# Performance work log

Measured on AMD Instinct MI355X. Metric: run time of the kernel, lower is better.

Reference implementation:

```python
import jax, jax.numpy as jnp
import numpy as np

NEG_SLOPE = 0.01  # nn.LeakyReLU default


def layer_norm(x, g, b, eps=1e-5):
    mu = x.mean(-1, keepdims=True)
    var = x.var(-1, keepdims=True)
    return (x - mu) / jnp.sqrt(var + eps) * g + b


def gru_layer(x, W_ih, W_hh, b_ih, b_hh):
    # x: (N, T, in). PyTorch GRU gate order: r, z, n.
    N, T, _ = x.shape
    H = W_hh.shape[1]
    xg = x @ W_ih.T + b_ih              # (N, T, 3H), input projections precomputed
    xg = jnp.transpose(xg, (1, 0, 2))   # (T, N, 3H)

    def step(h, xt):
        hg = h @ W_hh.T + b_hh
        xr, xz, xn = jnp.split(xt, 3, axis=-1)
        hr, hz, hn = jnp.split(hg, 3, axis=-1)
        r = jax.nn.sigmoid(xr + hr)
        z = jax.nn.sigmoid(xz + hz)
        n = jnp.tanh(xn + r * hn)
        h = (1.0 - z) * n + z * h
        return h, h

    h0 = jnp.zeros((N, H), x.dtype)
    _, ys = jax.lax.scan(step, h0, xg)  # (T, N, H)
    return jnp.transpose(ys, (1, 0, 2))


def prior_hconv(xW, Hinc):
    # PyG HypergraphConv: out = D_n^{-1} H B_e^{-1} H^T (x W^T); diag norms as vector scales
    d_n = Hinc.sum(1)
    d_e = Hinc.sum(0)
    inv_dn = jnp.where(d_n > 0, 1.0 / d_n, 0.0)
    inv_de = jnp.where(d_e > 0, 1.0 / d_e, 0.0)
    m = (Hinc.T @ xW) * inv_de[:, None]  # (E, H) hyperedge aggregation
    return (Hinc @ m) * inv_dn[:, None]


def soft_hconv(xW, Hinc):
    # SoftHypergraphConv: D_n^{-1/2} H D_e^{-1} H^T (x W^T + b)
    d_n = Hinc.sum(1)
    d_e = Hinc.sum(0)
    inv_sqrt_dn = jnp.where(d_n > 0, 1.0 / jnp.sqrt(d_n), 0.0)
    inv_de = jnp.where(d_e > 0, 1.0 / d_e, 0.0)
    m = (Hinc.T @ xW) * inv_de[:, None]
    return (Hinc @ m) * inv_sqrt_dn[:, None]


def setup_inputs() -> dict:
    key = jax.random.key(0)
    N, T, F, H, K, E = 4000, 64, 128, 128, 32, 64
    ks = jax.random.split(key, 20)
    s = 0.05
    inp = {
        'x': jax.random.normal(ks[0], (N, T, F), jnp.float32),
        'industry_matrix': jax.random.randint(ks[1], (N, E), 0, 2, jnp.int32),
        'ln_g': jnp.ones((F,), jnp.float32),
        'ln_b': jnp.zeros((F,), jnp.float32),
        'W_ih0': jax.random.normal(ks[2], (3 * H, F), jnp.float32) * s,
        'W_hh0': jax.random.normal(ks[3], (3 * H, H), jnp.float32) * s,
        'b_ih0': jax.random.normal(ks[4], (3 * H,), jnp.float32) * s,
        'b_hh0': jax.random.normal(ks[5], (3 * H,), jnp.float32) * s,
        'W_ih1': jax.random.normal(ks[6], (3 * H, H), jnp.float32) * s,
        'W_hh1': jax.random.normal(ks[7], (3 * H, H), jnp.float32) * s,
        'b_ih1': jax.random.normal(ks[8], (3 * H,), jnp.float32) * s,
        'b_hh1': jax.random.normal(ks[9], (3 * H,), jnp.float32) * s,
        'Wp': jax.random.normal(ks[10], (H, H), jnp.float32) * s,
        'bp': jax.random.normal(ks[11], (H,), jnp.float32) * s,
        'prototypes': jax.random.normal(ks[12], (K, H), jnp.float32),
        'Ws': jax.random.normal(ks[13], (H, H), jnp.float32) * s,
        'bs': jax.random.normal(ks[14], (H,), jnp.float32) * s,
        'Wa': jax.random.normal(ks[15], (H, H), jnp.float32) * s,
        'ba': jax.random.normal(ks[16], (H,), jnp.float32) * s,
        'Wf': jax.random.normal(ks[17], (1, 3 * H), jnp.float32) * s,
        'bf': jax.random.normal(ks[18], (1,), jnp.float32) * s,
    }
    return inp


def reference(x, industry_matrix, ln_g, ln_b, W_ih0, W_hh0, b_ih0, b_hh0,
              W_ih1, W_hh1, b_ih1, b_hh1, Wp, bp, prototypes, Ws, bs,
              Wa, ba, Wf, bf):
    lrelu = lambda v: jax.nn.leaky_relu(v, NEG_SLOPE)
    # FeatureExtractor: LN -> 2-layer GRU -> last timestep (linear branch is discarded in source)
    xn = layer_norm(x, ln_g, ln_b)
    h1 = gru_layer(xn, W_ih0, W_hh0, b_ih0, b_hh0)
    h2 = gru_layer(h1, W_ih1, W_hh1, b_ih1, b_hh1)
    e_s = h2[:, -1, :]                                   # (N, H)
    # PriorBetaModule: PyG HypergraphConv on binary industry incidence
    Hp = industry_matrix.astype(e_s.dtype)               # (N, E) 0/1 incidence
    e_p = lrelu(prior_hconv(e_s @ Wp.T, Hp) + bp)
    e_r = e_s - e_p
    # HiddenBetaModule: soft incidence via prototypes
    beta_h = jax.nn.sigmoid(e_r @ prototypes.T)          # (N, K)
    e_h = lrelu(soft_hconv(e_r @ Ws.T + bs, beta_h))
    e_residual = e_r - e_h
    e_alpha = lrelu(e_residual @ Wa.T + ba)
    out = jnp.concatenate([e_p, e_h, e_alpha], axis=1) @ Wf.T + bf
    return out.reshape(-1)                               # (N,)
```

## Files before the change

### kernel.cpp

```cpp
#include <hip/hip_runtime.h>
#include <hip/hip_fp16.h>

typedef float    f32x4 __attribute__((ext_vector_type(4)));
typedef _Float16 f16x8 __attribute__((ext_vector_type(8)));

__device__ __forceinline__ float sigmoidf_(float x) { return __builtin_amdgcn_rcpf(1.f + __expf(-x)); }
__device__ __forceinline__ float tanhf_(float x) { float e = __expf(2.f * x); return 1.f - 2.f * __builtin_amdgcn_rcpf(e + 1.f); }
__device__ __forceinline__ float lrelu_(float v) { return v > 0.f ? v : 0.01f * v; }

__device__ __forceinline__ f16x8 cvt8(const float* p) {
    const f32x4* q = (const f32x4*)p;
    f32x4 a = q[0], b = q[1];
    f16x8 v;
    v[0] = (_Float16)a[0]; v[1] = (_Float16)a[1]; v[2] = (_Float16)a[2]; v[3] = (_Float16)a[3];
    v[4] = (_Float16)b[0]; v[5] = (_Float16)b[1]; v[6] = (_Float16)b[2]; v[7] = (_Float16)b[3];
    return v;
}

__device__ __forceinline__ void gload_lds16(const void* g, void* l) {
    __builtin_amdgcn_global_load_lds(
        (const __attribute__((address_space(1))) void*)g,
        (__attribute__((address_space(3))) void*)l,
        16, 0, 0);
}

__global__ __launch_bounds__(256) void k_ln(const float* __restrict__ x,
                                            const float* __restrict__ g,
                                            const float* __restrict__ b,
                                            _Float16* __restrict__ xn, int N)
{
    int tid = threadIdx.x;
    int r = tid >> 4, i = tid & 15;
    size_t row = (size_t)blockIdx.x * 16 + r;
    int n = (int)(row >> 6), t = (int)(row & 63);
    const f32x4* xp = (const f32x4*)(x + row * 128 + i * 8);
    f32x4 a0 = xp[0], a1 = xp[1];
    float v0=a0[0], v1=a0[1], v2=a0[2], v3=a0[3], v4=a1[0], v5=a1[1], v6=a1[2], v7=a1[3];
    float s  = v0+v1+v2+v3+v4+v5+v6+v7;
    float s2 = v0*v0+v1*v1+v2*v2+v3*v3+v4*v4+v5*v5+v6*v6+v7*v7;
#pragma unroll
    for (int m = 1; m <= 8; m <<= 1) { s += __shfl_xor(s, m); s2 += __shfl_xor(s2, m); }
    float mu  = s * (1.f / 128.f);
    float var = s2 * (1.f / 128.f) - mu * mu;
    float rs  = rsqrtf(var + 1e-5f);
    const f32x4* gp = (const f32x4*)(g + i * 8);
    const f32x4* bp = (const f32x4*)(b + i * 8);
    f32x4 g0 = gp[0], g1 = gp[1], bb0 = bp[0], bb1 = bp[1];
    f16x8 o;
    o[0] = (_Float16)((v0 - mu) * rs * g0[0] + bb0[0]);
    o[1] = (_Float16)((v1 - mu) * rs * g0[1] + bb0[1]);
    o[2] = (_Float16)((v2 - mu) * rs * g0[2] + bb0[2]);
    o[3] = (_Float16)((v3 - mu) * rs * g0[3] + bb0[3]);
    o[4] = (_Float16)((v4 - mu) * rs * g1[0] + bb1[0]);
    o[5] = (_Float16)((v5 - mu) * rs * g1[1] + bb1[1]);
    o[6] = (_Float16)((v6 - mu) * rs * g1[2] + bb1[2]);
    o[7] = (_Float16)((v7 - mu) * rs * g1[3] + bb1[3]);
    *(f16x8*)(xn + ((size_t)t * N + n) * 128 + i * 8) = o;
}

__global__ __launch_bounds__(512) __attribute__((amdgpu_waves_per_eu(2)))
void k_gru2(const _Float16* __restrict__ xin,
            const float* __restrict__ W_ih0,
            const float* __restrict__ W_hh0,
            const float* __restrict__ b_ih0,
            const float* __restrict__ b_hh0,
            const float* __restrict__ W_ih1,
            const float* __restrict__ W_hh1,
            const float* __restrict__ b_ih1,
            const float* __restrict__ b_hh1,
            float* __restrict__ es, int N)
{
    __shared__ __align__(16) _Float16 wlds[96 * 64 * 8];
    __shared__ __align__(16) _Float16 wldsr[32 * 64 * 8];
    __shared__ __align__(16) _Float16 hbuf0[2][16 * 136];
    __shared__ __align__(16) _Float16 hbuf1[2][16 * 136];
    __shared__ __align__(16) _Float16 xls[2][16 * 128];

    int tid = threadIdx.x;
    int w = tid >> 6, lane = tid & 63;
    int ul = lane & 15, q = lane >> 4;
    int u = w * 16 + ul;
    int n0 = blockIdx.x * 16;

#pragma unroll
    for (int g = 0; g < 3; ++g)
#pragma unroll
        for (int kt = 0; kt < 4; ++kt) {
            f16x8 v = cvt8(W_ih0 + (size_t)(u + g * 128) * 128 + kt * 32 + q * 8);
            *(f16x8*)&wlds[(size_t)((w * 12 + g * 4 + kt) * 64 + lane) * 8] = v;
        }
#pragma unroll
    for (int kt = 0; kt < 4; ++kt) {
        f16x8 v = cvt8(W_hh0 + (size_t)u * 128 + kt * 32 + q * 8);
        *(f16x8*)&wldsr[(size_t)((w * 4 + kt) * 64 + lane) * 8] = v;
    }
    const _Float16* wbase  = &wlds[(size_t)(w * 12 * 64 + lane) * 8];
    const _Float16* w0base = &wldsr[(size_t)(w * 4 * 64 + lane) * 8];

    f16x8 whh0zn[8], wih1[12], whh1[12];
#pragma unroll
    for (int kt = 0; kt < 4; ++kt) {
        whh0zn[kt]     = cvt8(W_hh0 + (size_t)(u + 128) * 128 + kt * 32 + q * 8);
        whh0zn[4 + kt] = cvt8(W_hh0 + (size_t)(u + 256) * 128 + kt * 32 + q * 8);
    }
#pragma unroll
    for (int g = 0; g < 3; ++g)
#pragma unroll
        for (int kt = 0; kt < 4; ++kt) {
            size_t roff = (size_t)(u + g * 128) * 128 + kt * 32 + q * 8;
            wih1[g * 4 + kt] = cvt8(W_ih1 + roff);
            whh1[g * 4 + kt] = cvt8(W_hh1 + roff);
        }
    float br0 = b_ih0[u] + b_hh0[u], bz0 = b_ih0[u + 128] + b_hh0[u + 128];
    float bin0 = b_ih0[u + 256], bhn0 = b_hh0[u + 256];
    float br1 = b_ih1[u] + b_hh1[u], bz1 = b_ih1[u + 128] + b_hh1[u + 128];
    float bin1 = b_ih1[u + 256], bhn1 = b_hh1[u + 256];

    for (int idx = tid; idx < 16 * 136; idx += 512) {
        hbuf0[0][idx] = (_Float16)0.f;
        hbuf1[0][idx] = (_Float16)0.f;
        hbuf1[1][idx] = (_Float16)0.f;
    }
    float h0j[4] = {0.f, 0.f, 0.f, 0.f}, h1j[4] = {0.f, 0.f, 0.f, 0.f};
    const f32x4 Z4 = {0.f, 0.f, 0.f, 0.f};

    int xoff[4];
#pragma unroll
    for (int kt = 0; kt < 4; ++kt)
        xoff[kt] = (ul * 256 + kt * 64 + q * 16) ^ ((ul & 7) << 4);
    int dlin = w * 1024 + (lane << 4);
    int dsrc = dlin ^ (((dlin >> 8) & 7) << 4);

#define PREF_X(T, PB)                                                                \
    if (w < 4) {                                                                     \
        const char* gsrc = (const char*)(xin + ((size_t)(T) * N + n0) * 128);        \
        gload_lds16(gsrc + dsrc, (void*)((char*)&xls[PB][0] + dlin));                \
    }

#define LOAD_HF(HF, BUF, PB)                                                         \
    { const _Float16* hb = &BUF[PB][ul * 136 + q * 8];                               \
      _Pragma("unroll")                                                              \
      for (int kt = 0; kt < 4; ++kt) HF[kt] = *(const f16x8*)(hb + kt * 32); }

#define L0_KT(KT, XB)                                                                \
    {                                                                                \
        f16x8 xv  = *(const f16x8*)((XB) + xoff[KT]);                                \
        f16x8 wrv = *(const f16x8*)(wbase + (size_t)(KT) * 512);                     \
        f16x8 wzv = *(const f16x8*)(wbase + (size_t)(4 + (KT)) * 512);               \
        f16x8 wnv = *(const f16x8*)(wbase + (size_t)(8 + (KT)) * 512);               \
        f16x8 w0r = *(const f16x8*)(w0base + (size_t)(KT) * 512);                    \
        ar0  = __builtin_amdgcn_mfma_f32_16x16x32_f16(xv, wrv, ar0, 0, 0, 0);        \
        ar0  = __builtin_amdgcn_mfma_f32_16x16x32_f16(h0f[KT], w0r, ar0, 0, 0, 0);   \
        az0  = __builtin_amdgcn_mfma_f32_16x16x32_f16(xv, wzv, az0, 0, 0, 0);        \
        az0  = __builtin_amdgcn_mfma_f32_16x16x32_f16(h0f[KT], whh0zn[KT], az0, 0, 0, 0); \
        an0x = __builtin_amdgcn_mfma_f32_16x16x32_f16(xv, wnv, an0x, 0, 0, 0);       \
        an0h = __builtin_amdgcn_mfma_f32_16x16x32_f16(h0f[KT], whh0zn[4 + (KT)], an0h, 0, 0, 0); \
    }

#define L1_KT(KT)                                                                    \
    {                                                                                \
        ar1  = __builtin_amdgcn_mfma_f32_16x16x32_f16(h0f[KT], wih1[KT], ar1, 0, 0, 0); \
        ar1  = __builtin_amdgcn_mfma_f32_16x16x32_f16(h1f[KT], whh1[KT], ar1, 0, 0, 0); \
        az1  = __builtin_amdgcn_mfma_f32_16x16x32_f16(h0f[KT], wih1[4 + (KT)], az1, 0, 0, 0); \
        az1  = __builtin_amdgcn_mfma_f32_16x16x32_f16(h1f[KT], whh1[4 + (KT)], az1, 0, 0, 0); \
        an1x = __builtin_amdgcn_mfma_f32_16x16x32_f16(h0f[KT], wih1[8 + (KT)], an1x, 0, 0, 0); \
        an1h = __builtin_amdgcn_mfma_f32_16x16x32_f16(h1f[KT], whh1[8 + (KT)], an1h, 0, 0, 0); \
    }

#define GATES_L0(PW)                                                                 \
    { _Float16* wb = &hbuf0[PW][0];                                                  \
      _Pragma("unroll")                                                              \
      for (int j = 0; j < 4; ++j) {                                                  \
          float rr = sigmoidf_(ar0[j] + br0);                                        \
          float zz = sigmoidf_(az0[j] + bz0);                                        \
          float nn = tanhf_(an0x[j] + bin0 + rr * (an0h[j] + bhn0));                 \
          float hn = (1.f - zz) * nn + zz * h0j[j];                                  \
          h0j[j] = hn;                                                               \
          wb[(q * 4 + j) * 136 + u] = (_Float16)hn;                                  \
      } }

#define GATES_L1(PW)                                                                 \
    { _Float16* wb = &hbuf1[PW][0];                                                  \
      _Pragma("unroll")                                                              \
      for (int j = 0; j < 4; ++j) {                                                  \
          float rr = sigmoidf_(ar1[j] + br1);                                        \
          float zz = sigmoidf_(az1[j] + bz1);                                        \
          float nn = tanhf_(an1x[j] + bin1 + rr * (an1h[j] + bhn1));                 \
          float hn = (1.f - zz) * nn + zz * h1j[j];                                  \
          h1j[j] = hn;                                                               \
          wb[(q * 4 + j) * 136 + u] = (_Float16)hn;                                  \
      } }

    PREF_X(0, 0);
    __syncthreads();

    {
        PREF_X(1, 1);
        f16x8 h0f[4];
        LOAD_HF(h0f, hbuf0, 0);
        f32x4 ar0 = Z4, az0 = Z4, an0x = Z4, an0h = Z4;
        const char* xb = (const char*)&xls[0][0];
        L0_KT(0, xb) L0_KT(1, xb) L0_KT(2, xb) L0_KT(3, xb)
        GATES_L0(1);
        __syncthreads();
    }

    for (int s = 1; s < 64; ++s) {
        int P = s & 1;
        if (s < 63) { PREF_X(s + 1, P ^ 1); }
        f16x8 h0f[4], h1f[4];
        LOAD_HF(h0f, hbuf0, P);
        LOAD_HF(h1f, hbuf1, P);
        f32x4 ar0 = Z4, az0 = Z4, an0x = Z4, an0h = Z4;
        f32x4 ar1 = Z4, az1 = Z4, an1x = Z4, an1h = Z4;
        const char* xb = (const char*)&xls[P][0];
        L0_KT(0, xb) L1_KT(0)
        L0_KT(1, xb) L1_KT(1)
        L0_KT(2, xb) L1_KT(2)
        L0_KT(3, xb) L1_KT(3)
        GATES_L0(P ^ 1);
        GATES_L1(P ^ 1);
        __syncthreads();
    }

    {
        f16x8 h0f[4], h1f[4];
        LOAD_HF(h0f, hbuf0, 0);
        LOAD_HF(h1f, hbuf1, 0);
        f32x4 ar1 = Z4, az1 = Z4, an1x = Z4, an1h = Z4;
        L1_KT(0) L1_KT(1) L1_KT(2) L1_KT(3)
#pragma unroll
        for (int j = 0; j < 4; ++j) {
            float rr = sigmoidf_(ar1[j] + br1);
            float zz = sigmoidf_(az1[j] + bz1);
            float nn = tanhf_(an1x[j] + bin1 + rr * (an1h[j] + bhn1));
            h1j[j] = (1.f - zz) * nn + zz * h1j[j];
        }
    }

#pragma unroll
    for (int j = 0; j < 4; ++j)
        es[(size_t)(n0 + q * 4 + j) * 128 + u] = h1j[j];

#undef PREF_X
#undef LOAD_HF
#undef L0_KT
#undef L1_KT
#undef GATES_L0
#undef GATES_L1
}

#define STAGE_W(SRC)                                                                  \
    _Pragma("unroll")                                                                 \
    for (int tile = 0; tile < 2; ++tile)                                              \
    _Pragma("unroll")                                                                 \
    for (int kt = 0; kt < 4; ++kt) {                                                  \
        f16x8 v = cvt8((SRC) + (size_t)(w * 32 + tile * 16 + ul) * 128 + kt * 32 + q * 8); \
        *(f16x8*)&wfr[(size_t)(((w * 2 + tile) * 4 + kt) * 64 + lane) * 8] = v;       \
    }

#define LOAD_AF(AF, TF)                                                               \
    _Pragma("unroll")                                                                 \
    for (int kt = 0; kt < 4; ++kt) AF[kt] = cvt8(&TF[ul][kt * 32 + q * 8]);

#define MM128T(AF, A0, A1)                                                            \
    _Pragma("unroll")                                                                 \
    for (int kt = 0; kt < 4; ++kt) {                                                  \
        f16x8 b0 = *(const f16x8*)&wfr[(size_t)(((w * 2 + 0) * 4 + kt) * 64 + lane) * 8]; \
        f16x8 b1 = *(const f16x8*)&wfr[(size_t)(((w * 2 + 1) * 4 + kt) * 64 + lane) * 8]; \
        A0 = __builtin_amdgcn_mfma_f32_16x16x32_f16(AF[kt], b0, A0, 0, 0, 0);         \
        A1 = __builtin_amdgcn_mfma_f32_16x16x32_f16(AF[kt], b1, A1, 0, 0, 0);         \
    }

#define STAGE_ROWS16(DST, SRC)                                                        \
    { int r_ = tid >> 4, i_ = tid & 15;                                               \
      const f32x4* sp_ = (const f32x4*)((SRC) + (size_t)(n0 + r_) * 128 + i_ * 8);    \
      f32x4 a_ = sp_[0], b_ = sp_[1];                                                 \
      *(f32x4*)&DST[r_][i_ * 8] = a_;                                                 \
      *(f32x4*)&DST[r_][i_ * 8 + 4] = b_; }

__global__ __launch_bounds__(256) void k_postA(
    const float* __restrict__ e_s, const int* __restrict__ Hp,
    const float* __restrict__ Wp,
    float* __restrict__ macc_e, float* __restrict__ d_e)
{
    __shared__ __align__(16) _Float16 wfr[32 * 64 * 8];
    __shared__ float esf[16][132], xwf[16][132];
    int tid = threadIdx.x;
    int w = tid >> 6, lane = tid & 63;
    int ul = lane & 15, q = lane >> 4;
    int n0 = blockIdx.x * 16;
    const f32x4 Z4 = {0.f, 0.f, 0.f, 0.f};

    STAGE_W(Wp);
    STAGE_ROWS16(esf, e_s);
    __syncthreads();
    {
        f16x8 af[4]; LOAD_AF(af, esf);
        f32x4 a0 = Z4, a1 = Z4;
        MM128T(af, a0, a1);
#pragma unroll
        for (int j = 0; j < 4; ++j) {
            xwf[q * 4 + j][w * 32 + ul]      = a0[j];
            xwf[q * 4 + j][w * 32 + 16 + ul] = a1[j];
        }
    }
    __syncthreads();
    {
        int pair = tid >> 7, c = tid & 127;
        int js = pair * 32 + (lane & 31);
        float acc[32];
#pragma unroll
        for (int i = 0; i < 32; ++i) acc[i] = 0.f;
        float dcnt = 0.f;
        for (int r = 0; r < 16; ++r) {
            float sval = (float)Hp[(size_t)(n0 + r) * 64 + js];
            float xc = xwf[r][c];
            dcnt += sval;
            int sv = __float_as_int(sval);
#pragma unroll
            for (int jj = 0; jj < 32; ++jj)
                acc[jj] += __int_as_float(__builtin_amdgcn_readlane(sv, jj)) * xc;
        }
#pragma unroll
        for (int jj = 0; jj < 32; ++jj)
            atomicAdd(&macc_e[(size_t)(pair * 32 + jj) * 128 + c], acc[jj]);
        if ((w & 1) == 0 && (lane & 32) == 0)
            atomicAdd(&d_e[pair * 32 + lane], dcnt);
    }
}

__global__ __launch_bounds__(256) void k_postC(
    const float* __restrict__ e_s, const int* __restrict__ Hp,
    const float* __restrict__ bp, const float* __restrict__ prot,
    const float* __restrict__ Ws, const float* __restrict__ bs,
    const float* __restrict__ macc_e, const float* __restrict__ d_e,
    float* __restrict__ ep_g, float* __restrict__ er_g,
    float* __restrict__ beta_g, float* __restrict__ dn_g,
    float* __restrict__ macc_2, float* __restrict__ d_e2)
{
    __shared__ __align__(16) _Float16 wfr[32 * 64 * 8];
    __shared__ __align__(16) _Float16 pfr[8 * 64 * 8];
    __shared__ float mst[64 * 128];
    __shared__ float esf[16][132], erf[16][132], xwf[16][132];
    __shared__ float betaf[16][36];
    int tid = threadIdx.x;
    int w = tid >> 6, lane = tid & 63;
    int ul = lane & 15, q = lane >> 4;
    int n0 = blockIdx.x * 16;
    const f32x4 Z4 = {0.f, 0.f, 0.f, 0.f};

    for (int idx = tid; idx < 64 * 128; idx += 256) {
        float d = d_e[idx >> 7];
        mst[idx] = macc_e[idx] * (d > 0.f ? 1.f / d : 0.f);
    }
    STAGE_W(Ws);
    if (w < 2) {
#pragma unroll
        for (int kt = 0; kt < 4; ++kt) {
            f16x8 v = cvt8(prot + (size_t)(w * 16 + ul) * 128 + kt * 32 + q * 8);
            *(f16x8*)&pfr[(size_t)((w * 4 + kt) * 64 + lane) * 8] = v;
        }
    }
    STAGE_ROWS16(esf, e_s);
    __syncthreads();
    {
        int c = tid & 127, rh = tid >> 7;
        for (int rb = 0; rb < 8; ++rb) {
            int r = rb * 2 + rh;
            const int* hrow = Hp + (size_t)(n0 + r) * 64;
            float acc = 0.f, dsum = 0.f;
            for (int j = 0; j < 64; ++j) {
                float s = (float)hrow[j];
                dsum += s;
                acc += s * mst[j * 128 + c];
            }
            float inv = dsum > 0.f ? 1.f / dsum : 0.f;
            float v = lrelu_(acc * inv + bp[c]);
            float er = esf[r][c] - v;
            erf[r][c] = er;
            ep_g[(size_t)(n0 + r) * 128 + c] = v;
            er_g[(size_t)(n0 + r) * 128 + c] = er;
        }
    }
    __syncthreads();
    {
        f16x8 af[4]; LOAD_AF(af, erf);
        f32x4 a0 = Z4, a1 = Z4;
        MM128T(af, a0, a1);
        float bv0 = bs[w * 32 + ul], bv1 = bs[w * 32 + 16 + ul];
#pragma unroll
        for (int j = 0; j < 4; ++j) {
            xwf[q * 4 + j][w * 32 + ul]      = a0[j] + bv0;
            xwf[q * 4 + j][w * 32 + 16 + ul] = a1[j] + bv1;
        }
        if (w < 2) {
            f32x4 ab = Z4;
#pragma unroll
            for (int kt = 0; kt < 4; ++kt) {
                f16x8 bb = *(const f16x8*)&pfr[(size_t)((w * 4 + kt) * 64 + lane) * 8];
                ab = __builtin_amdgcn_mfma_f32_16x16x32_f16(af[kt], bb, ab, 0, 0, 0);
            }
#pragma unroll
            for (int j = 0; j < 4; ++j) {
                float s = sigmoidf_(ab[j]);
                betaf[q * 4 + j][w * 16 + ul] = s;
                beta_g[(size_t)(n0 + q * 4 + j) * 32 + w * 16 + ul] = s;
            }
        }
    }
    __syncthreads();
    if (tid < 16) {
        float s = 0.f;
        for (int k = 0; k < 32; ++k) s += betaf[tid][k];
        dn_g[n0 + tid] = s > 0.f ? rsqrtf(s) : 0.f;
    }
    {
        int pair = tid >> 7, c = tid & 127;
        float acc[32];
#pragma unroll
        for (int i = 0; i < 32; ++i) acc[i] = 0.f;
        float dcnt = 0.f;
        for (int r = pair; r < 16; r += 2) {
            float sval = betaf[r][lane & 31];
            float xc = xwf[r][c];
            dcnt += sval;
            int sv = __float_as_int(sval);
#pragma unroll
            for (int jj = 0; jj < 32; ++jj)
                acc[jj] += __int_as_float(__builtin_amdgcn_readlane(sv, jj)) * xc;
        }
#pragma unroll
        for (int jj = 0; jj < 32; ++jj)
            atomicAdd(&macc_2[(size_t)jj * 128 + c], acc[jj]);
        if ((w & 1) == 0 && (lane & 32) == 0)
            atomicAdd(&d_e2[lane], dcnt);
    }
}

__global__ __launch_bounds__(256) void k_postE(
    const float* __restrict__ ep_g, const float* __restrict__ er_g,
    const float* __restrict__ beta_g, const float* __restrict__ dn_g,
    const float* __restrict__ macc_2, const float* __restrict__ d_e2,
    const float* __restrict__ Wa, const float* __restrict__ ba,
    const float* __restrict__ Wf, const float* __restrict__ bf,
    float* __restrict__ out)
{
    __shared__ __align__(16) _Float16 wfr[32 * 64 * 8];
    __shared__ float mst[32 * 128];
    __shared__ float erf[16][132], ehf[16][132], ealf[16][132];
    __shared__ float betaf[16][36];
    __shared__ float dnf[16];
    int tid = threadIdx.x;
    int w = tid >> 6, lane = tid & 63;
    int ul = lane & 15, q = lane >> 4;
    int n0 = blockIdx.x * 16;
    const f32x4 Z4 = {0.f, 0.f, 0.f, 0.f};

    for (int idx = tid; idx < 32 * 128; idx += 256) {
        float d = d_e2[idx >> 7];
        mst[idx] = macc_2[idx] * (d > 0.f ? 1.f / d : 0.f);
    }
    STAGE_W(Wa);
    STAGE_ROWS16(erf, er_g);
    for (int idx = tid; idx < 16 * 32; idx += 256)
        betaf[idx >> 5][idx & 31] = beta_g[(size_t)(n0 + (idx >> 5)) * 32 + (idx & 31)];
    if (tid < 16) dnf[tid] = dn_g[n0 + tid];
    __syncthreads();
    {
        int c = tid & 127, rh = tid >> 7;
        for (int rb = 0; rb < 8; ++rb) {
            int r = rb * 2 + rh;
            float acc = 0.f;
            for (int j = 0; j < 32; ++j)
                acc += betaf[r][j] * mst[j * 128 + c];
            float v = lrelu_(acc * dnf[r]);
            ehf[r][c] = v;
            erf[r][c] = erf[r][c] - v;
        }
    }
    __syncthreads();
    {
        f16x8 af[4]; LOAD_AF(af, erf);
        f32x4 a0 = Z4, a1 = Z4;
        MM128T(af, a0, a1);
        float bv0 = ba[w * 32 + ul], bv1 = ba[w * 32 + 16 + ul];
#pragma unroll
        for (int j = 0; j < 4; ++j) {
            ealf[q * 4 + j][w * 32 + ul]      = lrelu_(a0[j] + bv0);
            ealf[q * 4 + j][w * 32 + 16 + ul] = lrelu_(a1[j] + bv1);
        }
    }
    __syncthreads();
    {
        int r = tid >> 4, i = tid & 15;
        float acc = 0.f;
#pragma unroll
        for (int kk = 0; kk < 8; ++kk) {
            int c = i * 8 + kk;
            acc += ep_g[(size_t)(n0 + r) * 128 + c] * Wf[c]
                 + ehf[r][c] * Wf[128 + c] + ealf[r][c] * Wf[256 + c];
        }
#pragma unroll
        for (int m = 1; m < 16; m <<= 1) acc += __shfl_xor(acc, m);
        if (i == 0) out[n0 + r] = acc + bf[0];
    }
}

extern "C" void kernel_launch(void* const* d_in, const int* in_sizes, int n_in,
                              void* d_out, int out_size, void* d_ws, size_t ws_size,
                              hipStream_t stream)
{
    const float* x     = (const float*)d_in[0];
    const int*   Hp    = (const int*)d_in[1];
    const float* ln_g  = (const float*)d_in[2];
    const float* ln_b  = (const float*)d_in[3];
    const float* W_ih0 = (const float*)d_in[4];
    const float* W_hh0 = (const float*)d_in[5];
    const float* b_ih0 = (const float*)d_in[6];
    const float* b_hh0 = (const float*)d_in[7];
    const float* W_ih1 = (const float*)d_in[8];
    const float* W_hh1 = (const float*)d_in[9];
    const float* b_ih1 = (const float*)d_in[10];
    const float* b_hh1 = (const float*)d_in[11];
    const float* Wp    = (const float*)d_in[12];
    const float* bp    = (const float*)d_in[13];
    const float* prot  = (const float*)d_in[14];
    const float* Ws    = (const float*)d_in[15];
    const float* bs    = (const float*)d_in[16];
    const float* Wa    = (const float*)d_in[17];
    const float* ba    = (const float*)d_in[18];
    const float* Wf    = (const float*)d_in[19];
    const float* bf    = (const float*)d_in[20];
    float* out = (float*)d_out;
    (void)n_in; (void)out_size; (void)ws_size;

    const int T = 64;
    int N = in_sizes[0] / (T * 128);
    size_t NT = (size_t)N * T;
    int NB = N / 16;

    char* ws = (char*)d_ws;
    size_t off = 0;
    auto alloc = [&](size_t bytes) { char* p = ws + off; off += (bytes + 255) & ~(size_t)255; return p; };
    _Float16* xn = (_Float16*)alloc(NT * 128 * 2);
    float* e_s   = (float*)alloc((size_t)N * 128 * 4);
    float* e_p   = (float*)alloc((size_t)N * 128 * 4);
    float* e_r   = (float*)alloc((size_t)N * 128 * 4);
    float* beta  = (float*)alloc((size_t)N * 32 * 4);
    float* dn    = (float*)alloc((size_t)N * 4);
    float* macc  = (float*)alloc((64 * 128 + 64 + 32 * 128 + 32) * 4);
    float* macc_e = macc;
    float* d_e    = macc + 64 * 128;
    float* macc_2 = d_e + 64;
    float* d_e2   = macc_2 + 32 * 128;

    k_ln<<<(int)(NT / 16), 256, 0, stream>>>(x, ln_g, ln_b, xn, N);
    k_gru2<<<NB, 512, 0, stream>>>(xn, W_ih0, W_hh0, b_ih0, b_hh0,
                                   W_ih1, W_hh1, b_ih1, b_hh1, e_s, N);

    hipMemsetAsync(macc, 0, (64 * 128 + 64 + 32 * 128 + 32) * 4, stream);

    k_postA<<<NB, 256, 0, stream>>>(e_s, Hp, Wp, macc_e, d_e);
    k_postC<<<NB, 256, 0, stream>>>(e_s, Hp, bp, prot, Ws, bs, macc_e, d_e,
                                    e_p, e_r, beta, dn, macc_2, d_e2);
    k_postE<<<NB, 256, 0, stream>>>(e_p, e_r, beta, dn, macc_2, d_e2,
                                    Wa, ba, Wf, bf, out);
}
```

Baseline: 432.5 us.

## Fuse post-GRU kernels into one persistent kernel with grid-wide barriers

The three post-processing kernels are merged into a single kernel that uses atomic-counter grid barriers between the hyperedge aggregation phases. Intermediate e_p, e_r, beta and dn now stay in shared memory instead of making a round trip through global memory. The separate memset is replaced by zeroing in block 0 of the layernorm kernel. This removes two launches, a memset and the global intermediate traffic. In exchange it relies on all 250 blocks being co-resident for the spin barrier, and shared-memory use per block grows, which lowers occupancy.

```diff
diff --git a/kernel.cpp b/kernel.cpp
--- a/kernel.cpp
+++ b/kernel.cpp
@@ -27,9 +27,13 @@
 __global__ __launch_bounds__(256) void k_ln(const float* __restrict__ x,
                                             const float* __restrict__ g,
                                             const float* __restrict__ b,
-                                            _Float16* __restrict__ xn, int N)
+                                            _Float16* __restrict__ xn, int N,
+                                            float* __restrict__ zbuf, int ztot)
 {
     int tid = threadIdx.x;
+    if (blockIdx.x == 0) {
+        for (int i = tid; i < ztot; i += 256) zbuf[i] = 0.f;
+    }
     int r = tid >> 4, i = tid & 15;
     size_t row = (size_t)blockIdx.x * 16 + r;
     int n = (int)(row >> 6), t = (int)(row & 63);
@@ -279,17 +283,46 @@
       *(f32x4*)&DST[r_][i_ * 8] = a_;                                                 \
       *(f32x4*)&DST[r_][i_ * 8 + 4] = b_; }
 
-__global__ __launch_bounds__(256) void k_postA(
+__device__ __forceinline__ void gsync(unsigned* cnt, unsigned target) {
+    __syncthreads();
+    if (threadIdx.x == 0) {
+        __threadfence();
+        atomicAdd(cnt, 1u);
+        while (__hip_atomic_load(cnt, __ATOMIC_ACQUIRE, __HIP_MEMORY_SCOPE_AGENT) < target)
+            __builtin_amdgcn_s_sleep(2);
+    }
+    __syncthreads();
+}
+
+__device__ __forceinline__ float gld(const float* p) {
+    return __hip_atomic_load(p, __ATOMIC_RELAXED, __HIP_MEMORY_SCOPE_AGENT);
+}
+
+__global__ __launch_bounds__(256) void k_postACE(
     const float* __restrict__ e_s, const int* __restrict__ Hp,
-    const float* __restrict__ Wp,
-    float* __restrict__ macc_e, float* __restrict__ d_e)
+    const float* __restrict__ Wp, const float* __restrict__ bp,
+    const float* __restrict__ prot,
+    const float* __restrict__ Ws, const float* __restrict__ bs,
+    const float* __restrict__ Wa, const float* __restrict__ ba,
+    const float* __restrict__ Wf, const float* __restrict__ bf,
+    float* __restrict__ macc_e, float* __restrict__ d_e,
+    float* __restrict__ macc_2, float* __restrict__ d_e2,
+    unsigned* __restrict__ cnt,
+    float* __restrict__ out)
 {
     __shared__ __align__(16) _Float16 wfr[32 * 64 * 8];
-    __shared__ float esf[16][132], xwf[16][132];
+    __shared__ __align__(16) _Float16 pfr[8 * 64 * 8];
+    __shared__ float mst[64 * 128];
+    __shared__ float esf[16][132], erf[16][132], epf[16][132];
+    __shared__ float xwf[16][132], ehf[16][132], ealf[16][132];
+    __shared__ float betaf[16][36];
+    __shared__ float dnf[16];
+
     int tid = threadIdx.x;
     int w = tid >> 6, lane = tid & 63;
     int ul = lane & 15, q = lane >> 4;
     int n0 = blockIdx.x * 16;
+    unsigned nb = gridDim.x;
     const f32x4 Z4 = {0.f, 0.f, 0.f, 0.f};
 
     STAGE_W(Wp);
@@ -328,31 +361,11 @@
         if ((w & 1) == 0 && (lane & 32) == 0)
             atomicAdd(&d_e[pair * 32 + lane], dcnt);
     }
-}
-
-__global__ __launch_bounds__(256) void k_postC(
-    const float* __restrict__ e_s, const int* __restrict__ Hp,
-    const float* __restrict__ bp, const float* __restrict__ prot,
-    const float* __restrict__ Ws, const float* __restrict__ bs,
-    const float* __restrict__ macc_e, const float* __restrict__ d_e,
-    float* __restrict__ ep_g, float* __restrict__ er_g,
-    float* __restrict__ beta_g, float* __restrict__ dn_g,
-    float* __restrict__ macc_2, float* __restrict__ d_e2)
-{
-    __shared__ __align__(16) _Float16 wfr[32 * 64 * 8];
-    __shared__ __align__(16) _Float16 pfr[8 * 64 * 8];
-    __shared__ float mst[64 * 128];
-    __shared__ float esf[16][132], erf[16][132], xwf[16][132];
-    __shared__ float betaf[16][36];
-    int tid = threadIdx.x;
-    int w = tid >> 6, lane = tid & 63;
-    int ul = lane & 15, q = lane >> 4;
-    int n0 = blockIdx.x * 16;
-    const f32x4 Z4 = {0.f, 0.f, 0.f, 0.f};
+    gsync(&cnt[0], nb);
 
     for (int idx = tid; idx < 64 * 128; idx += 256) {
-        float d = d_e[idx >> 7];
-        mst[idx] = macc_e[idx] * (d > 0.f ? 1.f / d : 0.f);
+        float d = gld(&d_e[idx >> 7]);
+        mst[idx] = gld(&macc_e[idx]) * (d > 0.f ? 1.f / d : 0.f);
     }
     STAGE_W(Ws);
     if (w < 2) {
@@ -362,7 +375,6 @@
             *(f16x8*)&pfr[(size_t)((w * 4 + kt) * 64 + lane) * 8] = v;
         }
     }
-    STAGE_ROWS16(esf, e_s);
     __syncthreads();
     {
         int c = tid & 127, rh = tid >> 7;
@@ -377,10 +389,8 @@
             }
             float inv = dsum > 0.f ? 1.f / dsum : 0.f;
             float v = lrelu_(acc * inv + bp[c]);
-            float er = esf[r][c] - v;
-            erf[r][c] = er;
-            ep_g[(size_t)(n0 + r) * 128 + c] = v;
-            er_g[(size_t)(n0 + r) * 128 + c] = er;
+            epf[r][c] = v;
+            erf[r][c] = esf[r][c] - v;
         }
     }
     __syncthreads();
@@ -402,18 +412,15 @@
                 ab = __builtin_amdgcn_mfma_f32_16x16x32_f16(af[kt], bb, ab, 0, 0, 0);
             }
 #pragma unroll
-            for (int j = 0; j < 4; ++j) {
-                float s = sigmoidf_(ab[j]);
-                betaf[q * 4 + j][w * 16 + ul] = s;
-                beta_g[(size_t)(n0 + q * 4 + j) * 32 + w * 16 + ul] = s;
-            }
+            for (int j = 0; j < 4; ++j)
+                betaf[q * 4 + j][w * 16 + ul] = sigmoidf_(ab[j]);
         }
     }
     __syncthreads();
     if (tid < 16) {
         float s = 0.f;
         for (int k = 0; k < 32; ++k) s += betaf[tid][k];
-        dn_g[n0 + tid] = s > 0.f ? rsqrtf(s) : 0.f;
+        dnf[tid] = s > 0.f ? rsqrtf(s) : 0.f;
     }
     {
         int pair = tid >> 7, c = tid & 127;
@@ -436,36 +443,13 @@
         if ((w & 1) == 0 && (lane & 32) == 0)
             atomicAdd(&d_e2[lane], dcnt);
     }
-}
-
-__global__ __launch_bounds__(256) void k_postE(
-    const float* __restrict__ ep_g, const float* __restrict__ er_g,
-    const float* __restrict__ beta_g, const float* __restrict__ dn_g,
-    const float* __restrict__ macc_2, const float* __restrict__ d_e2,
-    const float* __restrict__ Wa, const float* __restrict__ ba,
-    const float* __restrict__ Wf, const float* __restrict__ bf,
-    float* __restrict__ out)
-{
-    __shared__ __align__(16) _Float16 wfr[32 * 64 * 8];
-    __shared__ float mst[32 * 128];
-    __shared__ float erf[16][132], ehf[16][132], ealf[16][132];
-    __shared__ float betaf[16][36];
-    __shared__ float dnf[16];
-    int tid = threadIdx.x;
-    int w = tid >> 6, lane = tid & 63;
-    int ul = lane & 15, q = lane >> 4;
-    int n0 = blockIdx.x * 16;
-    const f32x4 Z4 = {0.f, 0.f, 0.f, 0.f};
+    gsync(&cnt[1], nb);
 
     for (int idx = tid; idx < 32 * 128; idx += 256) {
-        float d = d_e2[idx >> 7];
-        mst[idx] = macc_2[idx] * (d > 0.f ? 1.f / d : 0.f);
+        float d = gld(&d_e2[idx >> 7]);
+        mst[idx] = gld(&macc_2[idx]) * (d > 0.f ? 1.f / d : 0.f);
     }
     STAGE_W(Wa);
-    STAGE_ROWS16(erf, er_g);
-    for (int idx = tid; idx < 16 * 32; idx += 256)
-        betaf[idx >> 5][idx & 31] = beta_g[(size_t)(n0 + (idx >> 5)) * 32 + (idx & 31)];
-    if (tid < 16) dnf[tid] = dn_g[n0 + tid];
     __syncthreads();
     {
         int c = tid & 127, rh = tid >> 7;
@@ -498,8 +482,7 @@
 #pragma unroll
         for (int kk = 0; kk < 8; ++kk) {
             int c = i * 8 + kk;
-            acc += ep_g[(size_t)(n0 + r) * 128 + c] * Wf[c]
-                 + ehf[r][c] * Wf[128 + c] + ealf[r][c] * Wf[256 + c];
+            acc += epf[r][c] * Wf[c] + ehf[r][c] * Wf[128 + c] + ealf[r][c] * Wf[256 + c];
         }
 #pragma unroll
         for (int m = 1; m < 16; m <<= 1) acc += __shfl_xor(acc, m);
@@ -545,25 +528,17 @@
     auto alloc = [&](size_t bytes) { char* p = ws + off; off += (bytes + 255) & ~(size_t)255; return p; };
     _Float16* xn = (_Float16*)alloc(NT * 128 * 2);
     float* e_s   = (float*)alloc((size_t)N * 128 * 4);
-    float* e_p   = (float*)alloc((size_t)N * 128 * 4);
-    float* e_r   = (float*)alloc((size_t)N * 128 * 4);
-    float* beta  = (float*)alloc((size_t)N * 32 * 4);
-    float* dn    = (float*)alloc((size_t)N * 4);
-    float* macc  = (float*)alloc((64 * 128 + 64 + 32 * 128 + 32) * 4);
+    const int ZTOT = 64 * 128 + 64 + 32 * 128 + 32 + 8;
+    float* macc  = (float*)alloc((size_t)ZTOT * 4);
     float* macc_e = macc;
     float* d_e    = macc + 64 * 128;
     float* macc_2 = d_e + 64;
     float* d_e2   = macc_2 + 32 * 128;
-
-    k_ln<<<(int)(NT / 16), 256, 0, stream>>>(x, ln_g, ln_b, xn, N);
+    unsigned* cnt = (unsigned*)(d_e2 + 32);
+
+    k_ln<<<(int)(NT / 16), 256, 0, stream>>>(x, ln_g, ln_b, xn, N, macc, ZTOT);
     k_gru2<<<NB, 512, 0, stream>>>(xn, W_ih0, W_hh0, b_ih0, b_hh0,
                                    W_ih1, W_hh1, b_ih1, b_hh1, e_s, N);
-
-    hipMemsetAsync(macc, 0, (64 * 128 + 64 + 32 * 128 + 32) * 4, stream);
-
-    k_postA<<<NB, 256, 0, stream>>>(e_s, Hp, Wp, macc_e, d_e);
-    k_postC<<<NB, 256, 0, stream>>>(e_s, Hp, bp, prot, Ws, bs, macc_e, d_e,
-                                    e_p, e_r, beta, dn, macc_2, d_e2);
-    k_postE<<<NB, 256, 0, stream>>>(e_p, e_r, beta, dn, macc_2, d_e2,
-                                    Wa, ba, Wf, bf, out);
-}
+    k_postACE<<<NB, 256, 0, stream>>>(e_s, Hp, Wp, bp, prot, Ws, bs, Wa, ba, Wf, bf,
+                                      macc_e, d_e, macc_2, d_e2, cnt, out);
+}
```

Result: slower. 464.5 us (+7.4%).

## Split GRU layers across separate wave groups in a 1024-thread block

Applied to the files above, without the earlier changes.

The fused two-layer GRU kernel now runs with 1024 threads. Waves 0-7 compute layer 0 and waves 8-15 compute layer 1, pipelined one timestep apart, where before each wave computed both layers in sequence. The goal is to halve the serial MFMA chain per wave per step and spread the weight registers over more waves, so more of the recurrence latency is hidden. The cost is block-wide syncs across 16 waves, a larger block that may lower occupancy, and branch divergence between the two layer paths.

```diff
diff --git a/kernel.cpp b/kernel.cpp
--- a/kernel.cpp
+++ b/kernel.cpp
@@ -58,17 +58,16 @@
     *(f16x8*)(xn + ((size_t)t * N + n) * 128 + i * 8) = o;
 }
 
-__global__ __launch_bounds__(512) __attribute__((amdgpu_waves_per_eu(2)))
-void k_gru2(const _Float16* __restrict__ xin,
-            const float* __restrict__ W_ih0,
-            const float* __restrict__ W_hh0,
-            const float* __restrict__ b_ih0,
-            const float* __restrict__ b_hh0,
-            const float* __restrict__ W_ih1,
-            const float* __restrict__ W_hh1,
-            const float* __restrict__ b_ih1,
-            const float* __restrict__ b_hh1,
-            float* __restrict__ es, int N)
+__global__ __launch_bounds__(1024) void k_gru2(const _Float16* __restrict__ xin,
+                                               const float* __restrict__ W_ih0,
+                                               const float* __restrict__ W_hh0,
+                                               const float* __restrict__ b_ih0,
+                                               const float* __restrict__ b_hh0,
+                                               const float* __restrict__ W_ih1,
+                                               const float* __restrict__ W_hh1,
+                                               const float* __restrict__ b_ih1,
+                                               const float* __restrict__ b_hh1,
+                                               float* __restrict__ es, int N)
 {
     __shared__ __align__(16) _Float16 wlds[96 * 64 * 8];
     __shared__ __align__(16) _Float16 wldsr[32 * 64 * 8];
@@ -79,49 +78,53 @@
     int tid = threadIdx.x;
     int w = tid >> 6, lane = tid & 63;
     int ul = lane & 15, q = lane >> 4;
-    int u = w * 16 + ul;
+    int wl = w & 7;
+    int u = wl * 16 + ul;
+    bool isL0 = (w < 8);
     int n0 = blockIdx.x * 16;
 
+    if (isL0) {
+#pragma unroll
+        for (int g = 0; g < 3; ++g)
+#pragma unroll
+            for (int kt = 0; kt < 4; ++kt) {
+                f16x8 v = cvt8(W_ih0 + (size_t)(u + g * 128) * 128 + kt * 32 + q * 8);
+                *(f16x8*)&wlds[(size_t)((wl * 12 + g * 4 + kt) * 64 + lane) * 8] = v;
+            }
+    } else {
+#pragma unroll
+        for (int kt = 0; kt < 4; ++kt) {
+            f16x8 v = cvt8(W_ih1 + (size_t)(u + 256) * 128 + kt * 32 + q * 8);
+            *(f16x8*)&wldsr[(size_t)((wl * 4 + kt) * 64 + lane) * 8] = v;
+        }
+    }
+    const _Float16* wbase  = &wlds[(size_t)(wl * 12 * 64 + lane) * 8];
+    const _Float16* w1base = &wldsr[(size_t)(wl * 4 * 64 + lane) * 8];
+
+    const float* Wm = isL0 ? W_hh0 : W_hh1;
+    const float* W2 = isL0 ? W_hh0 : W_ih1;
+    f16x8 wreg[12], wreg2[8];
 #pragma unroll
     for (int g = 0; g < 3; ++g)
 #pragma unroll
-        for (int kt = 0; kt < 4; ++kt) {
-            f16x8 v = cvt8(W_ih0 + (size_t)(u + g * 128) * 128 + kt * 32 + q * 8);
-            *(f16x8*)&wlds[(size_t)((w * 12 + g * 4 + kt) * 64 + lane) * 8] = v;
-        }
+        for (int kt = 0; kt < 4; ++kt)
+            wreg[g * 4 + kt] = cvt8(Wm + (size_t)(u + g * 128) * 128 + kt * 32 + q * 8);
 #pragma unroll
     for (int kt = 0; kt < 4; ++kt) {
-        f16x8 v = cvt8(W_hh0 + (size_t)u * 128 + kt * 32 + q * 8);
-        *(f16x8*)&wldsr[(size_t)((w * 4 + kt) * 64 + lane) * 8] = v;
-    }
-    const _Float16* wbase  = &wlds[(size_t)(w * 12 * 64 + lane) * 8];
-    const _Float16* w0base = &wldsr[(size_t)(w * 4 * 64 + lane) * 8];
-
-    f16x8 whh0zn[8], wih1[12], whh1[12];
-#pragma unroll
-    for (int kt = 0; kt < 4; ++kt) {
-        whh0zn[kt]     = cvt8(W_hh0 + (size_t)(u + 128) * 128 + kt * 32 + q * 8);
-        whh0zn[4 + kt] = cvt8(W_hh0 + (size_t)(u + 256) * 128 + kt * 32 + q * 8);
-    }
-#pragma unroll
-    for (int g = 0; g < 3; ++g)
-#pragma unroll
-        for (int kt = 0; kt < 4; ++kt) {
-            size_t roff = (size_t)(u + g * 128) * 128 + kt * 32 + q * 8;
-            wih1[g * 4 + kt] = cvt8(W_ih1 + roff);
-            whh1[g * 4 + kt] = cvt8(W_hh1 + roff);
-        }
-    float br0 = b_ih0[u] + b_hh0[u], bz0 = b_ih0[u + 128] + b_hh0[u + 128];
-    float bin0 = b_ih0[u + 256], bhn0 = b_hh0[u + 256];
-    float br1 = b_ih1[u] + b_hh1[u], bz1 = b_ih1[u + 128] + b_hh1[u + 128];
-    float bin1 = b_ih1[u + 256], bhn1 = b_hh1[u + 256];
-
-    for (int idx = tid; idx < 16 * 136; idx += 512) {
+        wreg2[kt]     = cvt8(W2 + (size_t)u * 128 + kt * 32 + q * 8);
+        wreg2[4 + kt] = cvt8(W2 + (size_t)(u + 128) * 128 + kt * 32 + q * 8);
+    }
+    const float* bi = isL0 ? b_ih0 : b_ih1;
+    const float* bh = isL0 ? b_hh0 : b_hh1;
+    float br = bi[u] + bh[u], bz = bi[u + 128] + bh[u + 128];
+    float bin = bi[u + 256], bhn = bh[u + 256];
+
+    for (int idx = tid; idx < 16 * 136; idx += 1024) {
         hbuf0[0][idx] = (_Float16)0.f;
         hbuf1[0][idx] = (_Float16)0.f;
         hbuf1[1][idx] = (_Float16)0.f;
     }
-    float h0j[4] = {0.f, 0.f, 0.f, 0.f}, h1j[4] = {0.f, 0.f, 0.f, 0.f};
+    float hj[4] = {0.f, 0.f, 0.f, 0.f};
     const f32x4 Z4 = {0.f, 0.f, 0.f, 0.f};
 
     int xoff[4];
@@ -137,117 +140,79 @@
         gload_lds16(gsrc + dsrc, (void*)((char*)&xls[PB][0] + dlin));                \
     }
 
-#define LOAD_HF(HF, BUF, PB)                                                         \
-    { const _Float16* hb = &BUF[PB][ul * 136 + q * 8];                               \
-      _Pragma("unroll")                                                              \
-      for (int kt = 0; kt < 4; ++kt) HF[kt] = *(const f16x8*)(hb + kt * 32); }
-
-#define L0_KT(KT, XB)                                                                \
+#define COMPUTE(P)                                                                   \
     {                                                                                \
-        f16x8 xv  = *(const f16x8*)((XB) + xoff[KT]);                                \
-        f16x8 wrv = *(const f16x8*)(wbase + (size_t)(KT) * 512);                     \
-        f16x8 wzv = *(const f16x8*)(wbase + (size_t)(4 + (KT)) * 512);               \
-        f16x8 wnv = *(const f16x8*)(wbase + (size_t)(8 + (KT)) * 512);               \
-        f16x8 w0r = *(const f16x8*)(w0base + (size_t)(KT) * 512);                    \
-        ar0  = __builtin_amdgcn_mfma_f32_16x16x32_f16(xv, wrv, ar0, 0, 0, 0);        \
-        ar0  = __builtin_amdgcn_mfma_f32_16x16x32_f16(h0f[KT], w0r, ar0, 0, 0, 0);   \
-        az0  = __builtin_amdgcn_mfma_f32_16x16x32_f16(xv, wzv, az0, 0, 0, 0);        \
-        az0  = __builtin_amdgcn_mfma_f32_16x16x32_f16(h0f[KT], whh0zn[KT], az0, 0, 0, 0); \
-        an0x = __builtin_amdgcn_mfma_f32_16x16x32_f16(xv, wnv, an0x, 0, 0, 0);       \
-        an0h = __builtin_amdgcn_mfma_f32_16x16x32_f16(h0f[KT], whh0zn[4 + (KT)], an0h, 0, 0, 0); \
-    }
-
-#define L1_KT(KT)                                                                    \
-    {                                                                                \
-        ar1  = __builtin_amdgcn_mfma_f32_16x16x32_f16(h0f[KT], wih1[KT], ar1, 0, 0, 0); \
-        ar1  = __builtin_amdgcn_mfma_f32_16x16x32_f16(h1f[KT], whh1[KT], ar1, 0, 0, 0); \
-        az1  = __builtin_amdgcn_mfma_f32_16x16x32_f16(h0f[KT], wih1[4 + (KT)], az1, 0, 0, 0); \
-        az1  = __builtin_amdgcn_mfma_f32_16x16x32_f16(h1f[KT], whh1[4 + (KT)], az1, 0, 0, 0); \
-        an1x = __builtin_amdgcn_mfma_f32_16x16x32_f16(h0f[KT], wih1[8 + (KT)], an1x, 0, 0, 0); \
-        an1h = __builtin_amdgcn_mfma_f32_16x16x32_f16(h1f[KT], whh1[8 + (KT)], an1h, 0, 0, 0); \
-    }
-
-#define GATES_L0(PW)                                                                 \
-    { _Float16* wb = &hbuf0[PW][0];                                                  \
-      _Pragma("unroll")                                                              \
-      for (int j = 0; j < 4; ++j) {                                                  \
-          float rr = sigmoidf_(ar0[j] + br0);                                        \
-          float zz = sigmoidf_(az0[j] + bz0);                                        \
-          float nn = tanhf_(an0x[j] + bin0 + rr * (an0h[j] + bhn0));                 \
-          float hn = (1.f - zz) * nn + zz * h0j[j];                                  \
-          h0j[j] = hn;                                                               \
-          wb[(q * 4 + j) * 136 + u] = (_Float16)hn;                                  \
-      } }
-
-#define GATES_L1(PW)                                                                 \
-    { _Float16* wb = &hbuf1[PW][0];                                                  \
-      _Pragma("unroll")                                                              \
-      for (int j = 0; j < 4; ++j) {                                                  \
-          float rr = sigmoidf_(ar1[j] + br1);                                        \
-          float zz = sigmoidf_(az1[j] + bz1);                                        \
-          float nn = tanhf_(an1x[j] + bin1 + rr * (an1h[j] + bhn1));                 \
-          float hn = (1.f - zz) * nn + zz * h1j[j];                                  \
-          h1j[j] = hn;                                                               \
-          wb[(q * 4 + j) * 136 + u] = (_Float16)hn;                                  \
-      } }
+        f32x4 ar = Z4, az = Z4, anx = Z4, anh = Z4;                                  \
+        if (isL0) {                                                                  \
+            const char* xb = (const char*)&xls[P][0];                                \
+            const _Float16* hb = &hbuf0[P][ul * 136 + q * 8];                        \
+            _Pragma("unroll")                                                        \
+            for (int kt = 0; kt < 4; ++kt) {                                         \
+                f16x8 fa = *(const f16x8*)(xb + xoff[kt]);                           \
+                f16x8 fb = *(const f16x8*)(hb + kt * 32);                            \
+                f16x8 wrv = *(const f16x8*)(wbase + (size_t)(kt) * 512);             \
+                f16x8 wzv = *(const f16x8*)(wbase + (size_t)(4 + kt) * 512);         \
+                f16x8 wnv = *(const f16x8*)(wbase + (size_t)(8 + kt) * 512);         \
+                ar  = __builtin_amdgcn_mfma_f32_16x16x32_f16(fa, wrv, ar, 0, 0, 0);  \
+                az  = __builtin_amdgcn_mfma_f32_16x16x32_f16(fa, wzv, az, 0, 0, 0);  \
+                anx = __builtin_amdgcn_mfma_f32_16x16x32_f16(fa, wnv, anx, 0, 0, 0); \
+                ar  = __builtin_amdgcn_mfma_f32_16x16x32_f16(fb, wreg[kt], ar, 0, 0, 0); \
+                az  = __builtin_amdgcn_mfma_f32_16x16x32_f16(fb, wreg[4 + kt], az, 0, 0, 0); \
+                anh = __builtin_amdgcn_mfma_f32_16x16x32_f16(fb, wreg[8 + kt], anh, 0, 0, 0); \
+            }                                                                        \
+        } else {                                                                     \
+            const _Float16* ha = &hbuf0[P][ul * 136 + q * 8];                        \
+            const _Float16* hb = &hbuf1[P][ul * 136 + q * 8];                        \
+            _Pragma("unroll")                                                        \
+            for (int kt = 0; kt < 4; ++kt) {                                         \
+                f16x8 fa = *(const f16x8*)(ha + kt * 32);                            \
+                f16x8 fb = *(const f16x8*)(hb + kt * 32);                            \
+                f16x8 wnv = *(const f16x8*)(w1base + (size_t)(kt) * 512);            \
+                ar  = __builtin_amdgcn_mfma_f32_16x16x32_f16(fa, wreg2[kt], ar, 0, 0, 0); \
+                az  = __builtin_amdgcn_mfma_f32_16x16x32_f16(fa, wreg2[4 + kt], az, 0, 0, 0); \
+                anx = __builtin_amdgcn_mfma_f32_16x16x32_f16(fa, wnv, anx, 0, 0, 0); \
+                ar  = __builtin_amdgcn_mfma_f32_16x16x32_f16(fb, wreg[kt], ar, 0, 0, 0); \
+                az  = __builtin_amdgcn_mfma_f32_16x16x32_f16(fb, wreg[4 + kt], az, 0, 0, 0); \
+                anh = __builtin_amdgcn_mfma_f32_16x16x32_f16(fb, wreg[8 + kt], anh, 0, 0, 0); \
+            }                                                                        \
+        }                                                                            \
+        _Float16* wb = isL0 ? &hbuf0[(P) ^ 1][0] : &hbuf1[(P) ^ 1][0];               \
+        _Pragma("unroll")                                                            \
+        for (int j = 0; j < 4; ++j) {                                                \
+            float rr = sigmoidf_(ar[j] + br);                                        \
+            float zz = sigmoidf_(az[j] + bz);                                        \
+            float nn = tanhf_(anx[j] + bin + rr * (anh[j] + bhn));                   \
+            float hn = (1.f - zz) * nn + zz * hj[j];                                 \
+            hj[j] = hn;                                                              \
+            wb[(q * 4 + j) * 136 + u] = (_Float16)hn;                                \
+        }                                                                            \
+    }
 
     PREF_X(0, 0);
     __syncthreads();
 
     {
         PREF_X(1, 1);
-        f16x8 h0f[4];
-        LOAD_HF(h0f, hbuf0, 0);
-        f32x4 ar0 = Z4, az0 = Z4, an0x = Z4, an0h = Z4;
-        const char* xb = (const char*)&xls[0][0];
-        L0_KT(0, xb) L0_KT(1, xb) L0_KT(2, xb) L0_KT(3, xb)
-        GATES_L0(1);
+        if (isL0) COMPUTE(0);
         __syncthreads();
     }
 
     for (int s = 1; s < 64; ++s) {
         int P = s & 1;
         if (s < 63) { PREF_X(s + 1, P ^ 1); }
-        f16x8 h0f[4], h1f[4];
-        LOAD_HF(h0f, hbuf0, P);
-        LOAD_HF(h1f, hbuf1, P);
-        f32x4 ar0 = Z4, az0 = Z4, an0x = Z4, an0h = Z4;
-        f32x4 ar1 = Z4, az1 = Z4, an1x = Z4, an1h = Z4;
-        const char* xb = (const char*)&xls[P][0];
-        L0_KT(0, xb) L1_KT(0)
-        L0_KT(1, xb) L1_KT(1)
-        L0_KT(2, xb) L1_KT(2)
-        L0_KT(3, xb) L1_KT(3)
-        GATES_L0(P ^ 1);
-        GATES_L1(P ^ 1);
+        COMPUTE(P);
         __syncthreads();
     }
 
-    {
-        f16x8 h0f[4], h1f[4];
-        LOAD_HF(h0f, hbuf0, 0);
-        LOAD_HF(h1f, hbuf1, 0);
-        f32x4 ar1 = Z4, az1 = Z4, an1x = Z4, an1h = Z4;
-        L1_KT(0) L1_KT(1) L1_KT(2) L1_KT(3)
-#pragma unroll
-        for (int j = 0; j < 4; ++j) {
-            float rr = sigmoidf_(ar1[j] + br1);
-            float zz = sigmoidf_(az1[j] + bz1);
-            float nn = tanhf_(an1x[j] + bin1 + rr * (an1h[j] + bhn1));
-            h1j[j] = (1.f - zz) * nn + zz * h1j[j];
-        }
-    }
-
-#pragma unroll
-    for (int j = 0; j < 4; ++j)
-        es[(size_t)(n0 + q * 4 + j) * 128 + u] = h1j[j];
+    if (!isL0) {
+        COMPUTE(0);
+#pragma unroll
+        for (int j = 0; j < 4; ++j)
+            es[(size_t)(n0 + q * 4 + j) * 128 + u] = hj[j];
+    }
 
 #undef PREF_X
-#undef LOAD_HF
-#undef L0_KT
-#undef L1_KT
-#undef GATES_L0
-#undef GATES_L1
+#undef COMPUTE
 }
 
 #define STAGE_W(SRC)                                                                  \
@@ -556,8 +521,8 @@
     float* d_e2   = macc_2 + 32 * 128;
 
     k_ln<<<(int)(NT / 16), 256, 0, stream>>>(x, ln_g, ln_b, xn, N);
-    k_gru2<<<NB, 512, 0, stream>>>(xn, W_ih0, W_hh0, b_ih0, b_hh0,
-                                   W_ih1, W_hh1, b_ih1, b_hh1, e_s, N);
+    k_gru2<<<NB, 1024, 0, stream>>>(xn, W_ih0, W_hh0, b_ih0, b_hh0,
+                                    W_ih1, W_hh1, b_ih1, b_hh1, e_s, N);
 
     hipMemsetAsync(macc, 0, (64 * 128 + 64 + 32 * 128 + 32) * 4, stream);
 
```

New measurement: 444.4 us. +2.8%, slower.
